# Kernel tuning notes

Measured on AMD Instinct MI355X. Metric: run time of the kernel, lower is better.

Reference implementation:

```python
import jax, jax.numpy as jnp
import numpy as np

GROUPS = 32
EPS = 1e-6


def setup_inputs() -> dict:
    key = jax.random.key(0)
    ks = jax.random.split(key, 6)
    B, C, H, W = 2, 512, 64, 64
    s = 1.0 / np.sqrt(C)
    return {
        "x": jax.random.normal(ks[0], (B, C, H, W), dtype=jnp.float32),
        "gn_scale": jnp.ones((C,), dtype=jnp.float32),
        "gn_bias": jnp.zeros((C,), dtype=jnp.float32),
        "wq": jax.random.normal(ks[1], (C, C), dtype=jnp.float32) * s,
        "bq": jnp.zeros((C,), dtype=jnp.float32),
        "wk": jax.random.normal(ks[2], (C, C), dtype=jnp.float32) * s,
        "bk": jnp.zeros((C,), dtype=jnp.float32),
        "wv": jax.random.normal(ks[3], (C, C), dtype=jnp.float32) * s,
        "bv": jnp.zeros((C,), dtype=jnp.float32),
        "wp": jax.random.normal(ks[4], (C, C), dtype=jnp.float32) * s,
        "bp": jnp.zeros((C,), dtype=jnp.float32),
    }


def reference(x, gn_scale, gn_bias, wq, bq, wk, bk, wv, bv, wp, bp):
    B, C, H, W = x.shape
    N = H * W
    # GroupNorm(32, C, eps=1e-6) with affine, over (channels-per-group, H, W)
    g = x.reshape(B, GROUPS, C // GROUPS, N)
    mean = jnp.mean(g, axis=(2, 3), keepdims=True)
    var = jnp.var(g, axis=(2, 3), keepdims=True)
    h = ((g - mean) * jax.lax.rsqrt(var + EPS)).reshape(B, C, N)
    h = h * gn_scale[None, :, None] + gn_bias[None, :, None]
    # 1x1 convs == channel-wise linear maps; h is [B, C, N]
    q = jnp.einsum('oc,bcn->bon', wq, h) + bq[None, :, None]
    k = jnp.einsum('oc,bcn->bon', wk, h) + bk[None, :, None]
    v = jnp.einsum('oc,bcn->bon', wv, h) + bv[None, :, None]
    # full attention (chunking in original is a tiling detail; same math)
    scores = jnp.einsum('bci,bcj->bij', q, k) * (C ** -0.5)  # [B, N, N]
    attn = jax.nn.softmax(scores, axis=-1)
    out = jnp.einsum('bij,bcj->bci', attn, v)  # [B, C, N]
    hp = jnp.einsum('oc,bcn->bon', wp, out) + bp[None, :, None]
    return x + hp.reshape(B, C, H, W)
```

## Files before the change

### kernel.cpp

```cpp
#include <hip/hip_runtime.h>
#include <math.h>

#define BB 2
#define CC_ 512
#define GG 32
#define CG 16
#define NN 4096
#define NCH 4
#define EPSF 1e-6f
#define SCALEF 0.04419417382415922f

typedef unsigned short ushort_t;
typedef __bf16 bf16x8 __attribute__((ext_vector_type(8)));
typedef ushort_t ushortx8 __attribute__((ext_vector_type(8)));
typedef float floatx4 __attribute__((ext_vector_type(4)));

__device__ __forceinline__ ushort_t f2bf(float f) {
    union { float f; unsigned u; } x; x.f = f;
    unsigned r = (x.u + 0x7FFFu + ((x.u >> 16) & 1u)) >> 16;
    return (ushort_t)r;
}
__device__ __forceinline__ float bf2f(ushort_t v) {
    union { unsigned u; float f; } x; x.u = ((unsigned)v) << 16; return x.f;
}

__global__ __launch_bounds__(256) void gn_stats(const float* __restrict__ x,
                                                float* __restrict__ mv) {
    int bg = blockIdx.x;
    const float4* xp = (const float4*)(x + (size_t)bg * (CG * NN));
    float s = 0.f, ss = 0.f;
    for (int idx = threadIdx.x; idx < CG * NN / 4; idx += 256) {
        float4 v = xp[idx];
        s  += (v.x + v.y) + (v.z + v.w);
        ss += v.x * v.x + v.y * v.y + v.z * v.z + v.w * v.w;
    }
    __shared__ float sm[8];
    for (int off = 32; off > 0; off >>= 1) {
        s  += __shfl_down(s, off, 64);
        ss += __shfl_down(ss, off, 64);
    }
    int lane = threadIdx.x & 63, wv = threadIdx.x >> 6;
    if (lane == 0) { sm[wv] = s; sm[4 + wv] = ss; }
    __syncthreads();
    if (threadIdx.x == 0) {
        s  = sm[0] + sm[1] + sm[2] + sm[3];
        ss = sm[4] + sm[5] + sm[6] + sm[7];
        const float inv = 1.0f / (float)(CG * NN);
        float mean = s * inv;
        float var  = ss * inv - mean * mean;
        mv[bg]      = mean;
        mv[64 + bg] = rsqrtf(var + EPSF);
    }
}

__global__ __launch_bounds__(256) void gn_apply_t(const float* __restrict__ x,
                                                  const float* __restrict__ gamma,
                                                  const float* __restrict__ beta,
                                                  const float* __restrict__ mv,
                                                  ushort_t* __restrict__ hT) {
    const int b  = blockIdx.z;
    const int c0 = blockIdx.y * 64;
    const int n0 = blockIdx.x * 64;
    __shared__ float T[64][65];
    const int tid = threadIdx.x;
#pragma unroll
    for (int it = 0; it < 4; ++it) {
        int c  = it * 16 + (tid >> 4);
        int n4 = (tid & 15) * 4;
        int bg = b * 32 + ((c0 + c) >> 4);
        float a  = mv[64 + bg] * gamma[c0 + c];
        float b2 = beta[c0 + c] - mv[bg] * a;
        float4 v = *(const float4*)&x[((size_t)b * CC_ + c0 + c) * NN + n0 + n4];
        T[c][n4 + 0] = v.x * a + b2;
        T[c][n4 + 1] = v.y * a + b2;
        T[c][n4 + 2] = v.z * a + b2;
        T[c][n4 + 3] = v.w * a + b2;
    }
    __syncthreads();
#pragma unroll
    for (int it = 0; it < 4; ++it) {
        int n  = it * 16 + (tid >> 4);
        int c4 = (tid & 15) * 4;
        ushort4 u;
        u.x = f2bf(T[c4 + 0][n]); u.y = f2bf(T[c4 + 1][n]);
        u.z = f2bf(T[c4 + 2][n]); u.w = f2bf(T[c4 + 3][n]);
        *(ushort4*)&hT[((size_t)b * NN + n0 + n) * CC_ + c0 + c4] = u;
    }
}

template<int MODE>
__global__ __launch_bounds__(256) void conv_mfma(const ushort_t* __restrict__ Ain,
                                                 const float* __restrict__ W,
                                                 const float* __restrict__ bias,
                                                 const float* __restrict__ resid,
                                                 void* __restrict__ outv,
                                                 float oscale) {
    constexpr int ASTR = 40;
    constexpr size_t SMraw = (MODE == 2) ? (size_t)128 * 132 * 4
                          : (MODE == 1) ? (size_t)128 * 136 * 2
                                        : (size_t)2 * 128 * ASTR * 2;
    constexpr size_t SMEM = (SMraw > (size_t)2 * 128 * ASTR * 2) ? SMraw : (size_t)2 * 128 * ASTR * 2;
    __shared__ __align__(16) char smem[SMEM];
    ushort_t* At = (ushort_t*)smem;
    ushort_t* Bt = At + 128 * ASTR;

    const int b  = blockIdx.z;
    const int o0 = blockIdx.y * 128;
    const int n0 = blockIdx.x * 128;
    const ushort_t* Ab = Ain + (size_t)b * NN * CC_;
    const int tid = threadIdx.x;
    const int w = tid >> 6, lane = tid & 63, quad = lane >> 4, n16 = lane & 15;
    const int wm = w & 1, wn = w >> 1;
    const int r2 = tid >> 1, half = tid & 1;

    floatx4 acc[4][4];
#pragma unroll
    for (int i = 0; i < 4; ++i)
#pragma unroll
        for (int j = 0; j < 4; ++j) acc[i][j] = (floatx4){0.f, 0.f, 0.f, 0.f};

    for (int k0 = 0; k0 < CC_; k0 += 32) {
        const ushort_t* asrc = Ab + (size_t)(n0 + r2) * CC_ + k0 + half * 16;
        bf16x8 a0 = *(const bf16x8*)(asrc);
        bf16x8 a1 = *(const bf16x8*)(asrc + 8);
        const float* wsrc = W + (size_t)(o0 + r2) * CC_ + k0 + half * 16;
        float4 w0 = *(const float4*)(wsrc);
        float4 w1 = *(const float4*)(wsrc + 4);
        float4 w2 = *(const float4*)(wsrc + 8);
        float4 w3 = *(const float4*)(wsrc + 12);
        __syncthreads();
        *(bf16x8*)&At[r2 * ASTR + half * 16]     = a0;
        *(bf16x8*)&At[r2 * ASTR + half * 16 + 8] = a1;
        ushortx8 p0, p1;
        p0[0] = f2bf(w0.x); p0[1] = f2bf(w0.y); p0[2] = f2bf(w0.z); p0[3] = f2bf(w0.w);
        p0[4] = f2bf(w1.x); p0[5] = f2bf(w1.y); p0[6] = f2bf(w1.z); p0[7] = f2bf(w1.w);
        p1[0] = f2bf(w2.x); p1[1] = f2bf(w2.y); p1[2] = f2bf(w2.z); p1[3] = f2bf(w2.w);
        p1[4] = f2bf(w3.x); p1[5] = f2bf(w3.y); p1[6] = f2bf(w3.z); p1[7] = f2bf(w3.w);
        *(ushortx8*)&Bt[r2 * ASTR + half * 16]     = p0;
        *(ushortx8*)&Bt[r2 * ASTR + half * 16 + 8] = p1;
        __syncthreads();
        bf16x8 af[4], bf_[4];
#pragma unroll
        for (int mt = 0; mt < 4; ++mt)
            af[mt] = *(const bf16x8*)&At[(wm * 64 + mt * 16 + n16) * ASTR + quad * 8];
#pragma unroll
        for (int nt = 0; nt < 4; ++nt)
            bf_[nt] = *(const bf16x8*)&Bt[(wn * 64 + nt * 16 + n16) * ASTR + quad * 8];
#pragma unroll
        for (int mt = 0; mt < 4; ++mt)
#pragma unroll
            for (int nt = 0; nt < 4; ++nt)
                acc[mt][nt] = __builtin_amdgcn_mfma_f32_16x16x32_bf16(af[mt], bf_[nt], acc[mt][nt], 0, 0, 0);
    }

    float bsv[4];
#pragma unroll
    for (int nt = 0; nt < 4; ++nt) bsv[nt] = bias[o0 + wn * 64 + nt * 16 + n16];

    if (MODE == 0) {
        ushort_t* ob = (ushort_t*)outv + (size_t)b * NN * CC_;
#pragma unroll
        for (int mt = 0; mt < 4; ++mt)
#pragma unroll
            for (int nt = 0; nt < 4; ++nt) {
                int o = o0 + wn * 64 + nt * 16 + n16;
#pragma unroll
                for (int r = 0; r < 4; ++r) {
                    int n_sp = n0 + wm * 64 + mt * 16 + quad * 4 + r;
                    ob[(size_t)n_sp * CC_ + o] = f2bf((acc[mt][nt][r] + bsv[nt]) * oscale);
                }
            }
    } else if (MODE == 1) {
        __syncthreads();
        ushort_t* T = (ushort_t*)smem;
#pragma unroll
        for (int mt = 0; mt < 4; ++mt)
#pragma unroll
            for (int nt = 0; nt < 4; ++nt) {
                int ol = wn * 64 + nt * 16 + n16;
#pragma unroll
                for (int r = 0; r < 4; ++r) {
                    int nl = wm * 64 + mt * 16 + quad * 4 + r;
                    T[ol * 136 + nl] = f2bf(acc[mt][nt][r] + bsv[nt]);
                }
            }
        __syncthreads();
        ushort_t* ob = (ushort_t*)outv + (size_t)b * CC_ * NN;
#pragma unroll
        for (int i = 0; i < 8; ++i) {
            ushortx8 v = *(const ushortx8*)&T[r2 * 136 + half * 64 + i * 8];
            *(ushortx8*)&ob[(size_t)(o0 + r2) * NN + n0 + half * 64 + i * 8] = v;
        }
    } else {
        __syncthreads();
        float* Tf = (float*)smem;
#pragma unroll
        for (int mt = 0; mt < 4; ++mt)
#pragma unroll
            for (int nt = 0; nt < 4; ++nt) {
                int ol = wn * 64 + nt * 16 + n16;
#pragma unroll
                for (int r = 0; r < 4; ++r) {
                    int nl = wm * 64 + mt * 16 + quad * 4 + r;
                    Tf[ol * 132 + nl] = acc[mt][nt][r] + bsv[nt];
                }
            }
        __syncthreads();
        float* ob = (float*)outv + (size_t)b * CC_ * NN;
        const float* rb = resid + (size_t)b * CC_ * NN;
#pragma unroll
        for (int i = 0; i < 16; ++i) {
            float4 v  = *(const float4*)&Tf[r2 * 132 + half * 64 + i * 4];
            float4 x4 = *(const float4*)&rb[(size_t)(o0 + r2) * NN + n0 + half * 64 + i * 4];
            v.x += x4.x; v.y += x4.y; v.z += x4.z; v.w += x4.w;
            *(float4*)&ob[(size_t)(o0 + r2) * NN + n0 + half * 64 + i * 4] = v;
        }
    }
}

__global__ __launch_bounds__(512, 2) void flash_attn2(
        const ushort_t* __restrict__ qT, const ushort_t* __restrict__ kT,
        const ushort_t* __restrict__ vB,
        ushort_t* __restrict__ opart, float* __restrict__ lpart) {
    const int b     = blockIdx.z;
    const int chunk = blockIdx.y;
    const int i0    = blockIdx.x * 128;
    const ushort_t* qTb = qT + (size_t)b * NN * CC_;
    const ushort_t* kTb = kT + (size_t)b * NN * CC_;
    const ushort_t* vBb = vB + (size_t)b * CC_ * NN;

    __shared__ ushort_t Klds[64 * 520];
    __shared__ ushort_t Plds[128 * 72];

    const int tid  = threadIdx.x;
    const int w    = tid >> 6;
    const int lane = tid & 63;
    const int quad = lane >> 4;
    const int n16  = lane & 15;
    const int cb   = w * 64;

    bf16x8 aq[16];
    {
        const ushort_t* qrow = qTb + (size_t)(i0 + w * 16 + n16) * CC_ + quad * 8;
#pragma unroll
        for (int ks = 0; ks < 16; ++ks) aq[ks] = *(const bf16x8*)(qrow + ks * 32);
    }

    floatx4 acc[8][4];
#pragma unroll
    for (int mt = 0; mt < 8; ++mt)
#pragma unroll
        for (int st = 0; st < 4; ++st) acc[mt][st] = (floatx4){0.f, 0.f, 0.f, 0.f};
    float lsum[4] = {0.f, 0.f, 0.f, 0.f};

    const int jbase = chunk * (NN / NCH);
    for (int t = 0; t < (NN / NCH) / 64; ++t) {
        const int j0 = jbase + t * 64;
#pragma unroll
        for (int it = 0; it < 8; ++it) {
            int row = w * 8 + it;
            __builtin_amdgcn_global_load_lds(
                (const __attribute__((address_space(1))) unsigned int*)
                    (kTb + (size_t)(j0 + row) * CC_ + lane * 8),
                (__attribute__((address_space(3))) unsigned int*)(&Klds[row * 520]),
                16, 0, 0);
        }
        __syncthreads();

#pragma unroll
        for (int js = 0; js < 4; ++js) {
            floatx4 s = (floatx4){0.f, 0.f, 0.f, 0.f};
            const ushort_t* kb = &Klds[(js * 16 + n16) * 520 + quad * 8];
#pragma unroll
            for (int ks = 0; ks < 16; ++ks) {
                bf16x8 bk = *(const bf16x8*)(kb + ks * 32);
                s = __builtin_amdgcn_mfma_f32_16x16x32_bf16(aq[ks], bk, s, 0, 0, 0);
            }
            float e0 = __expf(s[0]), e1 = __expf(s[1]);
            float e2 = __expf(s[2]), e3 = __expf(s[3]);
            float p0 = e0, p1 = e1, p2 = e2, p3 = e3;
            p0 += __shfl_xor(p0, 1); p1 += __shfl_xor(p1, 1);
            p2 += __shfl_xor(p2, 1); p3 += __shfl_xor(p3, 1);
            p0 += __shfl_xor(p0, 2); p1 += __shfl_xor(p1, 2);
            p2 += __shfl_xor(p2, 2); p3 += __shfl_xor(p3, 2);
            p0 += __shfl_xor(p0, 4); p1 += __shfl_xor(p1, 4);
            p2 += __shfl_xor(p2, 4); p3 += __shfl_xor(p3, 4);
            p0 += __shfl_xor(p0, 8); p1 += __shfl_xor(p1, 8);
            p2 += __shfl_xor(p2, 8); p3 += __shfl_xor(p3, 8);
            lsum[0] += p0; lsum[1] += p1; lsum[2] += p2; lsum[3] += p3;
            const int pr = w * 16 + quad * 4;
            Plds[(pr + 0) * 72 + js * 16 + n16] = f2bf(e0);
            Plds[(pr + 1) * 72 + js * 16 + n16] = f2bf(e1);
            Plds[(pr + 2) * 72 + js * 16 + n16] = f2bf(e2);
            Plds[(pr + 3) * 72 + js * 16 + n16] = f2bf(e3);
        }
        __syncthreads();

        bf16x8 bv0[4], bv1[4];
#pragma unroll
        for (int st = 0; st < 4; ++st) {
            const ushort_t* vp = vBb + (size_t)(cb + st * 16 + n16) * NN + j0 + quad * 8;
            bv0[st] = *(const bf16x8*)(vp);
            bv1[st] = *(const bf16x8*)(vp + 32);
        }
#pragma unroll
        for (int mt = 0; mt < 8; ++mt) {
            const ushort_t* pr = &Plds[(mt * 16 + n16) * 72 + quad * 8];
            bf16x8 ap0 = *(const bf16x8*)(pr);
            bf16x8 ap1 = *(const bf16x8*)(pr + 32);
#pragma unroll
            for (int st = 0; st < 4; ++st) {
                acc[mt][st] = __builtin_amdgcn_mfma_f32_16x16x32_bf16(ap0, bv0[st], acc[mt][st], 0, 0, 0);
                acc[mt][st] = __builtin_amdgcn_mfma_f32_16x16x32_bf16(ap1, bv1[st], acc[mt][st], 0, 0, 0);
            }
        }
    }

    if (n16 == 0) {
        float* lp = lpart + ((size_t)b * NCH + chunk) * NN + i0 + w * 16 + quad * 4;
        lp[0] = lsum[0]; lp[1] = lsum[1]; lp[2] = lsum[2]; lp[3] = lsum[3];
    }
    ushort_t* opb = opart + ((size_t)b * NCH + chunk) * CC_ * NN;
#pragma unroll
    for (int mt = 0; mt < 8; ++mt)
#pragma unroll
        for (int st = 0; st < 4; ++st) {
            int c = cb + st * 16 + n16;
            int n = i0 + mt * 16 + quad * 4;
            ushort4 u;
            u.x = f2bf(acc[mt][st][0]); u.y = f2bf(acc[mt][st][1]);
            u.z = f2bf(acc[mt][st][2]); u.w = f2bf(acc[mt][st][3]);
            *(ushort4*)&opb[(size_t)c * NN + n] = u;
        }
}

__global__ __launch_bounds__(256) void combine(const ushort_t* __restrict__ opart,
                                               const float* __restrict__ lpart,
                                               ushort_t* __restrict__ attnT) {
    const int b  = blockIdx.z;
    const int c0 = blockIdx.y * 64;
    const int n0 = blockIdx.x * 64;
    __shared__ float S[64][65];
    const int tid = threadIdx.x;
#pragma unroll
    for (int it = 0; it < 4; ++it) {
        int c  = it * 16 + (tid >> 4);
        int n4 = (tid & 15) * 4;
        float s0 = 0.f, s1 = 0.f, s2 = 0.f, s3 = 0.f;
#pragma unroll
        for (int k = 0; k < NCH; ++k) {
            ushort4 u = *(const ushort4*)&opart[(((size_t)b * NCH + k) * CC_ + c0 + c) * NN + n0 + n4];
            s0 += bf2f(u.x); s1 += bf2f(u.y); s2 += bf2f(u.z); s3 += bf2f(u.w);
        }
        S[c][n4 + 0] = s0; S[c][n4 + 1] = s1; S[c][n4 + 2] = s2; S[c][n4 + 3] = s3;
    }
    __syncthreads();
#pragma unroll
    for (int it = 0; it < 4; ++it) {
        int n  = it * 16 + (tid >> 4);
        int c4 = (tid & 15) * 4;
        float l = 0.f;
#pragma unroll
        for (int k = 0; k < NCH; ++k) l += lpart[((size_t)b * NCH + k) * NN + n0 + n];
        float linv = 1.0f / l;
        ushort4 u;
        u.x = f2bf(S[c4 + 0][n] * linv); u.y = f2bf(S[c4 + 1][n] * linv);
        u.z = f2bf(S[c4 + 2][n] * linv); u.w = f2bf(S[c4 + 3][n] * linv);
        *(ushort4*)&attnT[((size_t)b * NN + n0 + n) * CC_ + c0 + c4] = u;
    }
}

extern "C" void kernel_launch(void* const* d_in, const int* in_sizes, int n_in,
                              void* d_out, int out_size, void* d_ws, size_t ws_size,
                              hipStream_t stream) {
    const float* x        = (const float*)d_in[0];
    const float* gn_scale = (const float*)d_in[1];
    const float* gn_bias  = (const float*)d_in[2];
    const float* wq = (const float*)d_in[3];
    const float* bq = (const float*)d_in[4];
    const float* wk = (const float*)d_in[5];
    const float* bk = (const float*)d_in[6];
    const float* wv = (const float*)d_in[7];
    const float* bv = (const float*)d_in[8];
    const float* wp = (const float*)d_in[9];
    const float* bp = (const float*)d_in[10];
    float* outp = (float*)d_out;

    const size_t TENS = (size_t)BB * CC_ * NN;
    ushort_t* hT    = (ushort_t*)d_ws;
    ushort_t* qT    = hT    + TENS;
    ushort_t* kT    = qT    + TENS;
    ushort_t* vB    = kT    + TENS;
    ushort_t* attnT = vB    + TENS;
    ushort_t* opart = attnT + TENS;
    float*    lpart = (float*)(opart + (size_t)NCH * TENS);
    float*    mv    = lpart + (size_t)BB * NCH * NN;

    gn_stats<<<BB * GG, 256, 0, stream>>>(x, mv);
    gn_apply_t<<<dim3(NN / 64, CC_ / 64, BB), 256, 0, stream>>>(x, gn_scale, gn_bias, mv, hT);

    dim3 cg(NN / 128, CC_ / 128, BB);
    conv_mfma<0><<<cg, 256, 0, stream>>>(hT, wq, bq, nullptr, (void*)qT, SCALEF);
    conv_mfma<0><<<cg, 256, 0, stream>>>(hT, wk, bk, nullptr, (void*)kT, 1.0f);
    conv_mfma<1><<<cg, 256, 0, stream>>>(hT, wv, bv, nullptr, (void*)vB, 1.0f);

    flash_attn2<<<dim3(NN / 128, NCH, BB), 512, 0, stream>>>(qT, kT, vB, opart, lpart);
    combine<<<dim3(NN / 64, CC_ / 64, BB), 256, 0, stream>>>(opart, lpart, attnT);

    conv_mfma<2><<<cg, 256, 0, stream>>>(attnT, wp, bp, x, (void*)outp, 1.0f);
}
```

Baseline: 324.5 us.

## Pre-convert weights, fuse QKV convs, retile attention and projection kernels

```diff
diff --git a/kernel.cpp b/kernel.cpp
--- a/kernel.cpp
+++ b/kernel.cpp
@@ -22,6 +22,23 @@
 }
 __device__ __forceinline__ float bf2f(ushort_t v) {
     union { unsigned u; float f; } x; x.u = ((unsigned)v) << 16; return x.f;
+}
+
+__global__ __launch_bounds__(256) void wprep(const float* __restrict__ wq,
+                                             const float* __restrict__ wk,
+                                             const float* __restrict__ wv,
+                                             const float* __restrict__ wp,
+                                             ushort_t* __restrict__ wqkv,
+                                             ushort_t* __restrict__ wpb) {
+    int idx4 = blockIdx.x * 256 + threadIdx.x;
+    int m = idx4 >> 16;
+    int r = idx4 & 65535;
+    const float* src = (m == 0) ? wq : (m == 1) ? wk : (m == 2) ? wv : wp;
+    float4 v = ((const float4*)src)[r];
+    ushort4 u;
+    u.x = f2bf(v.x); u.y = f2bf(v.y); u.z = f2bf(v.z); u.w = f2bf(v.w);
+    if (m < 3) ((ushort4*)wqkv)[(size_t)m * 65536 + r] = u;
+    else       ((ushort4*)wpb)[r] = u;
 }
 
 __global__ __launch_bounds__(256) void gn_stats(const float* __restrict__ x,
@@ -88,26 +105,23 @@
     }
 }
 
-template<int MODE>
-__global__ __launch_bounds__(256) void conv_mfma(const ushort_t* __restrict__ Ain,
-                                                 const float* __restrict__ W,
-                                                 const float* __restrict__ bias,
-                                                 const float* __restrict__ resid,
-                                                 void* __restrict__ outv,
-                                                 float oscale) {
+__global__ __launch_bounds__(256) void conv_qkv(const ushort_t* __restrict__ hT,
+                                                const ushort_t* __restrict__ wqkv,
+                                                const float* __restrict__ bq,
+                                                const float* __restrict__ bk,
+                                                const float* __restrict__ bv,
+                                                ushort_t* __restrict__ qT,
+                                                ushort_t* __restrict__ kT,
+                                                ushort_t* __restrict__ vB) {
     constexpr int ASTR = 40;
-    constexpr size_t SMraw = (MODE == 2) ? (size_t)128 * 132 * 4
-                          : (MODE == 1) ? (size_t)128 * 136 * 2
-                                        : (size_t)2 * 128 * ASTR * 2;
-    constexpr size_t SMEM = (SMraw > (size_t)2 * 128 * ASTR * 2) ? SMraw : (size_t)2 * 128 * ASTR * 2;
-    __shared__ __align__(16) char smem[SMEM];
+    __shared__ __align__(16) char smem[34816];
     ushort_t* At = (ushort_t*)smem;
     ushort_t* Bt = At + 128 * ASTR;
 
-    const int b  = blockIdx.z;
-    const int o0 = blockIdx.y * 128;
-    const int n0 = blockIdx.x * 128;
-    const ushort_t* Ab = Ain + (size_t)b * NN * CC_;
+    const int m0  = blockIdx.x * 128;
+    const int o0g = blockIdx.y * 128;
+    const int matid = o0g >> 9;
+    const int o0 = o0g & 511;
     const int tid = threadIdx.x;
     const int w = tid >> 6, lane = tid & 63, quad = lane >> 4, n16 = lane & 15;
     const int wm = w & 1, wn = w >> 1;
@@ -120,24 +134,17 @@
         for (int j = 0; j < 4; ++j) acc[i][j] = (floatx4){0.f, 0.f, 0.f, 0.f};
 
     for (int k0 = 0; k0 < CC_; k0 += 32) {
-        const ushort_t* asrc = Ab + (size_t)(n0 + r2) * CC_ + k0 + half * 16;
+        const ushort_t* asrc = &hT[(size_t)(m0 + r2) * CC_ + k0 + half * 16];
         bf16x8 a0 = *(const bf16x8*)(asrc);
         bf16x8 a1 = *(const bf16x8*)(asrc + 8);
-        const float* wsrc = W + (size_t)(o0 + r2) * CC_ + k0 + half * 16;
-        float4 w0 = *(const float4*)(wsrc);
-        float4 w1 = *(const float4*)(wsrc + 4);
-        float4 w2 = *(const float4*)(wsrc + 8);
-        float4 w3 = *(const float4*)(wsrc + 12);
+        const ushort_t* wsrc = &wqkv[(size_t)(o0g + r2) * CC_ + k0 + half * 16];
+        bf16x8 w0 = *(const bf16x8*)(wsrc);
+        bf16x8 w1 = *(const bf16x8*)(wsrc + 8);
         __syncthreads();
         *(bf16x8*)&At[r2 * ASTR + half * 16]     = a0;
         *(bf16x8*)&At[r2 * ASTR + half * 16 + 8] = a1;
-        ushortx8 p0, p1;
-        p0[0] = f2bf(w0.x); p0[1] = f2bf(w0.y); p0[2] = f2bf(w0.z); p0[3] = f2bf(w0.w);
-        p0[4] = f2bf(w1.x); p0[5] = f2bf(w1.y); p0[6] = f2bf(w1.z); p0[7] = f2bf(w1.w);
-        p1[0] = f2bf(w2.x); p1[1] = f2bf(w2.y); p1[2] = f2bf(w2.z); p1[3] = f2bf(w2.w);
-        p1[4] = f2bf(w3.x); p1[5] = f2bf(w3.y); p1[6] = f2bf(w3.z); p1[7] = f2bf(w3.w);
-        *(ushortx8*)&Bt[r2 * ASTR + half * 16]     = p0;
-        *(ushortx8*)&Bt[r2 * ASTR + half * 16 + 8] = p1;
+        *(bf16x8*)&Bt[r2 * ASTR + half * 16]     = w0;
+        *(bf16x8*)&Bt[r2 * ASTR + half * 16 + 8] = w1;
         __syncthreads();
         bf16x8 af[4], bf_[4];
 #pragma unroll
@@ -153,12 +160,14 @@
                 acc[mt][nt] = __builtin_amdgcn_mfma_f32_16x16x32_bf16(af[mt], bf_[nt], acc[mt][nt], 0, 0, 0);
     }
 
+    const float* bias = (matid == 0) ? bq : (matid == 1) ? bk : bv;
     float bsv[4];
 #pragma unroll
     for (int nt = 0; nt < 4; ++nt) bsv[nt] = bias[o0 + wn * 64 + nt * 16 + n16];
 
-    if (MODE == 0) {
-        ushort_t* ob = (ushort_t*)outv + (size_t)b * NN * CC_;
+    if (matid < 2) {
+        float scale = (matid == 0) ? SCALEF : 1.0f;
+        ushort_t* dst = (matid == 0) ? qT : kT;
 #pragma unroll
         for (int mt = 0; mt < 4; ++mt)
 #pragma unroll
@@ -166,11 +175,11 @@
                 int o = o0 + wn * 64 + nt * 16 + n16;
 #pragma unroll
                 for (int r = 0; r < 4; ++r) {
-                    int n_sp = n0 + wm * 64 + mt * 16 + quad * 4 + r;
-                    ob[(size_t)n_sp * CC_ + o] = f2bf((acc[mt][nt][r] + bsv[nt]) * oscale);
+                    int m = m0 + wm * 64 + mt * 16 + quad * 4 + r;
+                    dst[(size_t)m * CC_ + o] = f2bf((acc[mt][nt][r] + bsv[nt]) * scale);
                 }
             }
-    } else if (MODE == 1) {
+    } else {
         __syncthreads();
         ushort_t* T = (ushort_t*)smem;
 #pragma unroll
@@ -185,77 +194,56 @@
                 }
             }
         __syncthreads();
-        ushort_t* ob = (ushort_t*)outv + (size_t)b * CC_ * NN;
+        const int bb = m0 >> 12;
+        const int n0 = m0 & (NN - 1);
 #pragma unroll
         for (int i = 0; i < 8; ++i) {
             ushortx8 v = *(const ushortx8*)&T[r2 * 136 + half * 64 + i * 8];
-            *(ushortx8*)&ob[(size_t)(o0 + r2) * NN + n0 + half * 64 + i * 8] = v;
-        }
-    } else {
-        __syncthreads();
-        float* Tf = (float*)smem;
-#pragma unroll
-        for (int mt = 0; mt < 4; ++mt)
-#pragma unroll
-            for (int nt = 0; nt < 4; ++nt) {
-                int ol = wn * 64 + nt * 16 + n16;
-#pragma unroll
-                for (int r = 0; r < 4; ++r) {
-                    int nl = wm * 64 + mt * 16 + quad * 4 + r;
-                    Tf[ol * 132 + nl] = acc[mt][nt][r] + bsv[nt];
-                }
-            }
-        __syncthreads();
-        float* ob = (float*)outv + (size_t)b * CC_ * NN;
-        const float* rb = resid + (size_t)b * CC_ * NN;
-#pragma unroll
-        for (int i = 0; i < 16; ++i) {
-            float4 v  = *(const float4*)&Tf[r2 * 132 + half * 64 + i * 4];
-            float4 x4 = *(const float4*)&rb[(size_t)(o0 + r2) * NN + n0 + half * 64 + i * 4];
-            v.x += x4.x; v.y += x4.y; v.z += x4.z; v.w += x4.w;
-            *(float4*)&ob[(size_t)(o0 + r2) * NN + n0 + half * 64 + i * 4] = v;
-        }
-    }
-}
-
-__global__ __launch_bounds__(512, 2) void flash_attn2(
+            *(ushortx8*)&vB[((size_t)bb * CC_ + o0 + r2) * NN + n0 + half * 64 + i * 8] = v;
+        }
+    }
+}
+
+__global__ __launch_bounds__(256, 3) void flash_attn3(
         const ushort_t* __restrict__ qT, const ushort_t* __restrict__ kT,
         const ushort_t* __restrict__ vB,
         ushort_t* __restrict__ opart, float* __restrict__ lpart) {
     const int b     = blockIdx.z;
     const int chunk = blockIdx.y;
-    const int i0    = blockIdx.x * 128;
+    const int i0    = blockIdx.x * 32;
     const ushort_t* qTb = qT + (size_t)b * NN * CC_;
     const ushort_t* kTb = kT + (size_t)b * NN * CC_;
     const ushort_t* vBb = vB + (size_t)b * CC_ * NN;
 
-    __shared__ ushort_t Klds[64 * 520];
-    __shared__ ushort_t Plds[128 * 72];
+    __shared__ ushort_t Klds[32 * 520];
+    __shared__ ushort_t Plds[32 * 40];
 
     const int tid  = threadIdx.x;
     const int w    = tid >> 6;
     const int lane = tid & 63;
     const int quad = lane >> 4;
     const int n16  = lane & 15;
-    const int cb   = w * 64;
+    const int qt   = w & 1;
+    const int kh   = w >> 1;
+    const int cb   = w * 128;
 
     bf16x8 aq[16];
     {
-        const ushort_t* qrow = qTb + (size_t)(i0 + w * 16 + n16) * CC_ + quad * 8;
+        const ushort_t* qrow = qTb + (size_t)(i0 + qt * 16 + n16) * CC_ + quad * 8;
 #pragma unroll
         for (int ks = 0; ks < 16; ++ks) aq[ks] = *(const bf16x8*)(qrow + ks * 32);
     }
 
-    floatx4 acc[8][4];
-#pragma unroll
-    for (int mt = 0; mt < 8; ++mt)
-#pragma unroll
-        for (int st = 0; st < 4; ++st) acc[mt][st] = (floatx4){0.f, 0.f, 0.f, 0.f};
+    floatx4 acc[2][8];
+#pragma unroll
+    for (int mt = 0; mt < 2; ++mt)
+#pragma unroll
+        for (int st = 0; st < 8; ++st) acc[mt][st] = (floatx4){0.f, 0.f, 0.f, 0.f};
     float lsum[4] = {0.f, 0.f, 0.f, 0.f};
 
     const int jbase = chunk * (NN / NCH);
-    for (int t = 0; t < (NN / NCH) / 64; ++t) {
-        const int j0 = jbase + t * 64;
+    for (int t = 0; t < (NN / NCH) / 32; ++t) {
+        const int j0 = jbase + t * 32;
 #pragma unroll
         for (int it = 0; it < 8; ++it) {
             int row = w * 8 + it;
@@ -267,17 +255,19 @@
         }
         __syncthreads();
 
-#pragma unroll
-        for (int js = 0; js < 4; ++js) {
-            floatx4 s = (floatx4){0.f, 0.f, 0.f, 0.f};
-            const ushort_t* kb = &Klds[(js * 16 + n16) * 520 + quad * 8];
-#pragma unroll
-            for (int ks = 0; ks < 16; ++ks) {
-                bf16x8 bk = *(const bf16x8*)(kb + ks * 32);
-                s = __builtin_amdgcn_mfma_f32_16x16x32_bf16(aq[ks], bk, s, 0, 0, 0);
-            }
-            float e0 = __expf(s[0]), e1 = __expf(s[1]);
-            float e2 = __expf(s[2]), e3 = __expf(s[3]);
+        floatx4 sa = (floatx4){0.f, 0.f, 0.f, 0.f};
+        floatx4 sb = (floatx4){0.f, 0.f, 0.f, 0.f};
+        const ushort_t* kb = &Klds[(kh * 16 + n16) * 520 + quad * 8];
+#pragma unroll
+        for (int ks = 0; ks < 8; ++ks) {
+            bf16x8 k0 = *(const bf16x8*)(kb + (2 * ks) * 32);
+            bf16x8 k1 = *(const bf16x8*)(kb + (2 * ks + 1) * 32);
+            sa = __builtin_amdgcn_mfma_f32_16x16x32_bf16(aq[2 * ks],     k0, sa, 0, 0, 0);
+            sb = __builtin_amdgcn_mfma_f32_16x16x32_bf16(aq[2 * ks + 1], k1, sb, 0, 0, 0);
+        }
+        float e0 = __expf(sa[0] + sb[0]), e1 = __expf(sa[1] + sb[1]);
+        float e2 = __expf(sa[2] + sb[2]), e3 = __expf(sa[3] + sb[3]);
+        {
             float p0 = e0, p1 = e1, p2 = e2, p3 = e3;
             p0 += __shfl_xor(p0, 1); p1 += __shfl_xor(p1, 1);
             p2 += __shfl_xor(p2, 1); p3 += __shfl_xor(p3, 1);
@@ -288,43 +278,33 @@
             p0 += __shfl_xor(p0, 8); p1 += __shfl_xor(p1, 8);
             p2 += __shfl_xor(p2, 8); p3 += __shfl_xor(p3, 8);
             lsum[0] += p0; lsum[1] += p1; lsum[2] += p2; lsum[3] += p3;
-            const int pr = w * 16 + quad * 4;
-            Plds[(pr + 0) * 72 + js * 16 + n16] = f2bf(e0);
-            Plds[(pr + 1) * 72 + js * 16 + n16] = f2bf(e1);
-            Plds[(pr + 2) * 72 + js * 16 + n16] = f2bf(e2);
-            Plds[(pr + 3) * 72 + js * 16 + n16] = f2bf(e3);
-        }
-        __syncthreads();
-
-        bf16x8 bv0[4], bv1[4];
-#pragma unroll
-        for (int st = 0; st < 4; ++st) {
-            const ushort_t* vp = vBb + (size_t)(cb + st * 16 + n16) * NN + j0 + quad * 8;
-            bv0[st] = *(const bf16x8*)(vp);
-            bv1[st] = *(const bf16x8*)(vp + 32);
-        }
-#pragma unroll
-        for (int mt = 0; mt < 8; ++mt) {
-            const ushort_t* pr = &Plds[(mt * 16 + n16) * 72 + quad * 8];
-            bf16x8 ap0 = *(const bf16x8*)(pr);
-            bf16x8 ap1 = *(const bf16x8*)(pr + 32);
-#pragma unroll
-            for (int st = 0; st < 4; ++st) {
-                acc[mt][st] = __builtin_amdgcn_mfma_f32_16x16x32_bf16(ap0, bv0[st], acc[mt][st], 0, 0, 0);
-                acc[mt][st] = __builtin_amdgcn_mfma_f32_16x16x32_bf16(ap1, bv1[st], acc[mt][st], 0, 0, 0);
-            }
+        }
+        const int pr = qt * 16 + quad * 4;
+        Plds[(pr + 0) * 40 + kh * 16 + n16] = f2bf(e0);
+        Plds[(pr + 1) * 40 + kh * 16 + n16] = f2bf(e1);
+        Plds[(pr + 2) * 40 + kh * 16 + n16] = f2bf(e2);
+        Plds[(pr + 3) * 40 + kh * 16 + n16] = f2bf(e3);
+        __syncthreads();
+
+        bf16x8 ap0 = *(const bf16x8*)&Plds[n16 * 40 + quad * 8];
+        bf16x8 ap1 = *(const bf16x8*)&Plds[(16 + n16) * 40 + quad * 8];
+#pragma unroll
+        for (int st = 0; st < 8; ++st) {
+            bf16x8 bv8 = *(const bf16x8*)(vBb + (size_t)(cb + st * 16 + n16) * NN + j0 + quad * 8);
+            acc[0][st] = __builtin_amdgcn_mfma_f32_16x16x32_bf16(ap0, bv8, acc[0][st], 0, 0, 0);
+            acc[1][st] = __builtin_amdgcn_mfma_f32_16x16x32_bf16(ap1, bv8, acc[1][st], 0, 0, 0);
         }
     }
 
     if (n16 == 0) {
-        float* lp = lpart + ((size_t)b * NCH + chunk) * NN + i0 + w * 16 + quad * 4;
+        float* lp = lpart + (((size_t)b * NCH + chunk) * 2 + kh) * NN + i0 + qt * 16 + quad * 4;
         lp[0] = lsum[0]; lp[1] = lsum[1]; lp[2] = lsum[2]; lp[3] = lsum[3];
     }
     ushort_t* opb = opart + ((size_t)b * NCH + chunk) * CC_ * NN;
 #pragma unroll
-    for (int mt = 0; mt < 8; ++mt)
-#pragma unroll
-        for (int st = 0; st < 4; ++st) {
+    for (int mt = 0; mt < 2; ++mt)
+#pragma unroll
+        for (int st = 0; st < 8; ++st) {
             int c = cb + st * 16 + n16;
             int n = i0 + mt * 16 + quad * 4;
             ushort4 u;
@@ -361,12 +341,100 @@
         int c4 = (tid & 15) * 4;
         float l = 0.f;
 #pragma unroll
-        for (int k = 0; k < NCH; ++k) l += lpart[((size_t)b * NCH + k) * NN + n0 + n];
+        for (int k = 0; k < NCH * 2; ++k)
+            l += lpart[(((size_t)b * NCH) * 2 + k) * NN + n0 + n];
         float linv = 1.0f / l;
         ushort4 u;
         u.x = f2bf(S[c4 + 0][n] * linv); u.y = f2bf(S[c4 + 1][n] * linv);
         u.z = f2bf(S[c4 + 2][n] * linv); u.w = f2bf(S[c4 + 3][n] * linv);
         *(ushort4*)&attnT[((size_t)b * NN + n0 + n) * CC_ + c0 + c4] = u;
+    }
+}
+
+__global__ __launch_bounds__(256) void conv_proj(const ushort_t* __restrict__ attnT,
+                                                 const ushort_t* __restrict__ wpb,
+                                                 const float* __restrict__ bp,
+                                                 const float* __restrict__ x,
+                                                 float* __restrict__ out) {
+    constexpr int ASTR = 40;
+    __shared__ __align__(16) char smem[33792];
+    ushort_t* At = (ushort_t*)smem;
+    ushort_t* Bt = At + 128 * ASTR;
+
+    const int m0 = blockIdx.x * 128;
+    const int o0 = blockIdx.y * 64;
+    const int tid = threadIdx.x;
+    const int w = tid >> 6, lane = tid & 63, quad = lane >> 4, n16 = lane & 15;
+    const int wm = w & 1, wn = w >> 1;
+    const int r2 = tid >> 1, half = tid & 1;
+
+    floatx4 acc[4][2];
+#pragma unroll
+    for (int i = 0; i < 4; ++i)
+#pragma unroll
+        for (int j = 0; j < 2; ++j) acc[i][j] = (floatx4){0.f, 0.f, 0.f, 0.f};
+
+    for (int k0 = 0; k0 < CC_; k0 += 32) {
+        const ushort_t* asrc = &attnT[(size_t)(m0 + r2) * CC_ + k0 + half * 16];
+        bf16x8 a0 = *(const bf16x8*)(asrc);
+        bf16x8 a1 = *(const bf16x8*)(asrc + 8);
+        bf16x8 w0, w1;
+        if (tid < 128) {
+            const ushort_t* wsrc = &wpb[(size_t)(o0 + r2) * CC_ + k0 + half * 16];
+            w0 = *(const bf16x8*)(wsrc);
+            w1 = *(const bf16x8*)(wsrc + 8);
+        }
+        __syncthreads();
+        *(bf16x8*)&At[r2 * ASTR + half * 16]     = a0;
+        *(bf16x8*)&At[r2 * ASTR + half * 16 + 8] = a1;
+        if (tid < 128) {
+            *(bf16x8*)&Bt[r2 * ASTR + half * 16]     = w0;
+            *(bf16x8*)&Bt[r2 * ASTR + half * 16 + 8] = w1;
+        }
+        __syncthreads();
+        bf16x8 af[4], bf_[2];
+#pragma unroll
+        for (int mt = 0; mt < 4; ++mt)
+            af[mt] = *(const bf16x8*)&At[(wm * 64 + mt * 16 + n16) * ASTR + quad * 8];
+#pragma unroll
+        for (int nt = 0; nt < 2; ++nt)
+            bf_[nt] = *(const bf16x8*)&Bt[(wn * 32 + nt * 16 + n16) * ASTR + quad * 8];
+#pragma unroll
+        for (int mt = 0; mt < 4; ++mt)
+#pragma unroll
+            for (int nt = 0; nt < 2; ++nt)
+                acc[mt][nt] = __builtin_amdgcn_mfma_f32_16x16x32_bf16(af[mt], bf_[nt], acc[mt][nt], 0, 0, 0);
+    }
+
+    float bsv[2];
+#pragma unroll
+    for (int nt = 0; nt < 2; ++nt) bsv[nt] = bp[o0 + wn * 32 + nt * 16 + n16];
+
+    __syncthreads();
+    float* Tf = (float*)smem;
+#pragma unroll
+    for (int mt = 0; mt < 4; ++mt)
+#pragma unroll
+        for (int nt = 0; nt < 2; ++nt) {
+            int ol = wn * 32 + nt * 16 + n16;
+#pragma unroll
+            for (int r = 0; r < 4; ++r) {
+                int nl = wm * 64 + mt * 16 + quad * 4 + r;
+                Tf[ol * 132 + nl] = acc[mt][nt][r] + bsv[nt];
+            }
+        }
+    __syncthreads();
+    const int bb = m0 >> 12;
+    const int n0 = m0 & (NN - 1);
+    const int ro = tid >> 2;
+    const int cc = (tid & 3) * 32;
+    const size_t obase = ((size_t)bb * CC_ + o0 + ro) * NN + n0 + cc;
+#pragma unroll
+    for (int i = 0; i < 8; ++i) {
+        float4 v  = *(const float4*)&Tf[ro * 132 + cc + i * 4];
+        float4 x4 = *(const float4*)&x[obase + i * 4];
+        v.x += x4.x; v.y += x4.y; v.z += x4.z; v.w += x4.w;
+        *(float4*)&out[obase + i * 4] = v;
     }
 }
 
@@ -393,19 +461,20 @@
     ushort_t* vB    = kT    + TENS;
     ushort_t* attnT = vB    + TENS;
     ushort_t* opart = attnT + TENS;
-    float*    lpart = (float*)(opart + (size_t)NCH * TENS);
-    float*    mv    = lpart + (size_t)BB * NCH * NN;
-
+    ushort_t* wqkv  = opart + (size_t)NCH * TENS;
+    ushort_t* wpb   = wqkv  + (size_t)1536 * 512;
+    float*    lpart = (float*)(wpb + (size_t)512 * 512);
+    float*    mv    = lpart + (size_t)BB * NCH * 2 * NN;
+
+    wprep<<<1024, 256, 0, stream>>>(wq, wk, wv, wp, wqkv, wpb);
     gn_stats<<<BB * GG, 256, 0, stream>>>(x, mv);
     gn_apply_t<<<dim3(NN / 64, CC_ / 64, BB), 256, 0, stream>>>(x, gn_scale, gn_bias, mv, hT);
 
-    dim3 cg(NN / 128, CC_ / 128, BB);
-    conv_mfma<0><<<cg, 256, 0, stream>>>(hT, wq, bq, nullptr, (void*)qT, SCALEF);
-    conv_mfma<0><<<cg, 256, 0, stream>>>(hT, wk, bk, nullptr, (void*)kT, 1.0f);
-    conv_mfma<1><<<cg, 256, 0, stream>>>(hT, wv, bv, nullptr, (void*)vB, 1.0f);
-
-    flash_attn2<<<dim3(NN / 128, NCH, BB), 512, 0, stream>>>(qT, kT, vB, opart, lpart);
+    conv_qkv<<<dim3(BB * NN / 128, 1536 / 128), 256, 0, stream>>>(
+        hT, wqkv, bq, bk, bv, qT, kT, vB);
+
+    flash_attn3<<<dim3(NN / 32, NCH, BB), 256, 0, stream>>>(qT, kT, vB, opart, lpart);
     combine<<<dim3(NN / 64, CC_ / 64, BB), 256, 0, stream>>>(opart, lpart, attnT);
 
-    conv_mfma<2><<<cg, 256, 0, stream>>>(attnT, wp, bp, x, (void*)outp, 1.0f);
-}
+    conv_proj<<<dim3(BB * NN / 128, CC_ / 64), 256, 0, stream>>>(attnT, wpb, bp, x, outp);
+}
```

Measured after the change: 454.3 us. 1.4x slower.
